# Optimization experiments

Measured on AMD Instinct MI355X. Metric: run time of the kernel, lower is better.

The kernel has to match this reference:

```python
import jax, jax.numpy as jnp
import numpy as np

N = 50000      # nodes
E = 400000     # edges (before self loops)
IN = 128       # in_feat
HID = 64       # n_hidden per head
HEADS = [4, 4, 1]
NEG_SLOPE = 0.2  # DGL GATConv default


def gat_layer(h, src, dst, W, al, ar, b, n_nodes):
    # h: [N, Din]; W: [Din, H*F]; al/ar: [H, F]; b: [H*F]
    H, F = al.shape
    feat = (h @ W).reshape(n_nodes, H, F)              # [N,H,F]
    el = jnp.sum(feat * al, axis=-1)                   # [N,H]
    er = jnp.sum(feat * ar, axis=-1)                   # [N,H]
    e = jax.nn.leaky_relu(el[src] + er[dst], NEG_SLOPE)  # [E,H]
    # edge softmax over destination node segments (stable)
    e_max = jax.lax.stop_gradient(jax.ops.segment_max(e, dst, num_segments=n_nodes))
    ex = jnp.exp(e - e_max[dst])                       # [E,H]
    denom = jax.ops.segment_sum(ex, dst, num_segments=n_nodes)  # [N,H]
    alpha = ex / denom[dst]                            # [E,H]
    msg = feat[src] * alpha[:, :, None]                # [E,H,F]
    out = jax.ops.segment_sum(msg, dst, num_segments=n_nodes)   # [N,H,F]
    out = out + b.reshape(1, H, F)
    return out.reshape(n_nodes, H * F)


def setup_inputs() -> dict:
    key = jax.random.key(0)
    ks = jax.random.split(key, 16)
    inp = {
        "node_feat": jax.random.normal(ks[0], (N, IN), jnp.float32),
        "src": jax.random.randint(ks[1], (E,), 0, N),
        "dst": jax.random.randint(ks[2], (E,), 0, N),
    }
    dins = [IN, HID * HEADS[0], HID * HEADS[1]]
    for i, (din, h) in enumerate(zip(dins, HEADS)):
        k = 3 + 3 * i
        inp[f"W{i}"] = jax.random.normal(ks[k], (din, h * HID), jnp.float32) * 0.1
        inp[f"al{i}"] = jax.random.normal(ks[k + 1], (h, HID), jnp.float32) * 0.1
        inp[f"ar{i}"] = jax.random.normal(ks[k + 2], (h, HID), jnp.float32) * 0.1
        inp[f"b{i}"] = jnp.zeros((h * HID,), jnp.float32)
    return inp


def reference(node_feat, src, dst, W0, al0, ar0, b0, W1, al1, ar1, b1, W2, al2, ar2, b2):
    n_nodes = node_feat.shape[0]
    # add_self_loop
    loop = jnp.arange(n_nodes, dtype=src.dtype)
    src_a = jnp.concatenate([src, loop])
    dst_a = jnp.concatenate([dst, loop])
    h = node_feat
    h = gat_layer(h, src_a, dst_a, W0, al0, ar0, b0, n_nodes)  # [N, 4*64]
    h = gat_layer(h, src_a, dst_a, W1, al1, ar1, b1, n_nodes)  # [N, 4*64]
    h = gat_layer(h, src_a, dst_a, W2, al2, ar2, b2, n_nodes)  # [N, 64]
    return h
```

## Files before the change

### kernel.cpp

```cpp
#include <hip/hip_runtime.h>


typedef __attribute__((ext_vector_type(8))) short short8;
typedef __attribute__((ext_vector_type(4))) float f32x4;

__device__ __forceinline__ float bf2f(ushort u) {
  union { unsigned int i; float f; } c;
  c.i = ((unsigned int)u) << 16;
  return c.f;
}
__device__ __forceinline__ ushort f2bf(float f) {
  union { float f; unsigned int i; } c;
  c.f = f;
  unsigned int u = c.i;
  u += 0x7FFFu + ((u >> 16) & 1u);
  return (ushort)(u >> 16);
}
__device__ __forceinline__ float lrelu_exp(float x) {
  const float y = fmaxf(x, 0.2f * x);
  return __expf(y);
}
__device__ __forceinline__ void gload_lds16(const ushort* g, void* lds) {
  __builtin_amdgcn_global_load_lds(
      (const __attribute__((address_space(1))) unsigned int*)g,
      (__attribute__((address_space(3))) unsigned int*)lds, 16, 0, 0);
}

__global__ __launch_bounds__(256) void cvt_f32_bf16(const float* __restrict__ in,
                                                    ushort* __restrict__ out,
                                                    int n8) {
  const int i = blockIdx.x * 256 + threadIdx.x;
  if (i >= n8) return;
  const float4 v0 = ((const float4*)in)[i * 2];
  const float4 v1 = ((const float4*)in)[i * 2 + 1];
  short8 o;
  o[0] = (short)f2bf(v0.x); o[1] = (short)f2bf(v0.y);
  o[2] = (short)f2bf(v0.z); o[3] = (short)f2bf(v0.w);
  o[4] = (short)f2bf(v1.x); o[5] = (short)f2bf(v1.y);
  o[6] = (short)f2bf(v1.z); o[7] = (short)f2bf(v1.w);
  ((short8*)out)[i] = o;
}

__global__ void convert_w_kernel(const float* __restrict__ W,
                                 ushort* __restrict__ Wt, int K, int N) {
  const int i = blockIdx.x * 256 + threadIdx.x;
  if (i >= K * N) return;
  const int k = i / N, n = i - k * N;
  Wt[n * K + k] = f2bf(W[i]);
}

template <int BN>
__global__ __launch_bounds__(256) void gemm_mfma(
    const ushort* __restrict__ A, const ushort* __restrict__ Wt,
    ushort* __restrict__ C, int M, int K, int Nc) {
  constexpr int NF = BN / 32;
  __shared__ ushort As[128][32];
  __shared__ ushort Bs[BN][32];
  const int bm = blockIdx.x * 128;
  const int bn = blockIdx.y * BN;
  const int tid = threadIdx.x;
  const int lane = tid & 63;
  const int wave = tid >> 6;
  const int wm = wave >> 1;
  const int wn = wave & 1;

  f32x4 acc[4][NF];
#pragma unroll
  for (int m = 0; m < 4; ++m)
#pragma unroll
    for (int n = 0; n < NF; ++n) acc[m][n] = 0.f;

  for (int k0 = 0; k0 < K; k0 += 32) {
#pragma unroll
    for (int c = wave; c < 8; c += 4) {
      const int row = c * 16 + (lane >> 2);
      int rg = bm + row;
      if (rg >= M) rg = M - 1;
      gload_lds16(A + (size_t)rg * K + k0 + (lane & 3) * 8,
                  (char*)(&As[0][0]) + c * 1024);
    }
#pragma unroll
    for (int c = wave; c < BN / 16; c += 4) {
      const int row = c * 16 + (lane >> 2);
      gload_lds16(Wt + (size_t)(bn + row) * K + k0 + (lane & 3) * 8,
                  (char*)(&Bs[0][0]) + c * 1024);
    }
    __syncthreads();

    short8 a[4], b[NF];
#pragma unroll
    for (int m = 0; m < 4; ++m)
      a[m] = *(const short8*)&As[wm * 64 + m * 16 + (lane & 15)][(lane >> 4) * 8];
#pragma unroll
    for (int n = 0; n < NF; ++n)
      b[n] = *(const short8*)&Bs[wn * (NF * 16) + n * 16 + (lane & 15)]
                             [(lane >> 4) * 8];
#pragma unroll
    for (int m = 0; m < 4; ++m)
#pragma unroll
      for (int n = 0; n < NF; ++n)
        acc[m][n] = __builtin_amdgcn_mfma_f32_16x16x32_bf16(a[m], b[n],
                                                            acc[m][n], 0, 0, 0);
    __syncthreads();
  }

#pragma unroll
  for (int m = 0; m < 4; ++m) {
#pragma unroll
    for (int r = 0; r < 4; ++r) {
      const int row = bm + wm * 64 + m * 16 + (lane >> 4) * 4 + r;
      if (row < M) {
#pragma unroll
        for (int n = 0; n < NF; ++n) {
          const int col = bn + wn * (NF * 16) + n * 16 + (lane & 15);
          C[(size_t)row * Nc + col] = f2bf(acc[m][n][r]);
        }
      }
    }
  }
}

__global__ __launch_bounds__(256) void attn_coef_h4(
    const ushort* __restrict__ feat, const float* __restrict__ al,
    const float* __restrict__ ar, float* __restrict__ el,
    float* __restrict__ er, int Nn) {
  if (blockIdx.x == 0 && threadIdx.x < 4) el[Nn * 4 + threadIdx.x] = -1e9f;
  const int n = (blockIdx.x * 256 + threadIdx.x) >> 6;
  const int lane = threadIdx.x & 63;
  if (n >= Nn) return;
  const short4 v = ((const short4*)(feat + (size_t)n * 256))[lane];
  const float4 a = ((const float4*)al)[lane];
  const float4 r = ((const float4*)ar)[lane];
  const float f0 = bf2f((ushort)v.x), f1 = bf2f((ushort)v.y),
              f2 = bf2f((ushort)v.z), f3 = bf2f((ushort)v.w);
  float pl = f0 * a.x + f1 * a.y + f2 * a.z + f3 * a.w;
  float pr = f0 * r.x + f1 * r.y + f2 * r.z + f3 * r.w;
#pragma unroll
  for (int off = 1; off < 16; off <<= 1) {
    pl += __shfl_xor(pl, off);
    pr += __shfl_xor(pr, off);
  }
  if ((lane & 15) == 0) {
    el[n * 4 + (lane >> 4)] = pl;
    er[n * 4 + (lane >> 4)] = pr;
  }
}

__global__ __launch_bounds__(256) void attn_coef_h1(
    const ushort* __restrict__ feat, const float* __restrict__ al,
    const float* __restrict__ ar, float* __restrict__ el,
    float* __restrict__ er, int Nn) {
  if (blockIdx.x == 0 && threadIdx.x == 0) el[Nn] = -1e9f;
  const int wid = (blockIdx.x * 256 + threadIdx.x) >> 6;
  const int lane = threadIdx.x & 63;
  const int n = wid * 4 + (lane >> 4);
  const int sub = lane & 15;
  if (n >= Nn) return;
  const short4 v = ((const short4*)(feat + (size_t)n * 64))[sub];
  const float4 a = ((const float4*)al)[sub];
  const float4 r = ((const float4*)ar)[sub];
  const float f0 = bf2f((ushort)v.x), f1 = bf2f((ushort)v.y),
              f2 = bf2f((ushort)v.z), f3 = bf2f((ushort)v.w);
  float pl = f0 * a.x + f1 * a.y + f2 * a.z + f3 * a.w;
  float pr = f0 * r.x + f1 * r.y + f2 * r.z + f3 * r.w;
#pragma unroll
  for (int off = 1; off < 16; off <<= 1) {
    pl += __shfl_xor(pl, off);
    pr += __shfl_xor(pr, off);
  }
  if (sub == 0) {
    el[n] = pl;
    er[n] = pr;
  }
}

__global__ void hist_kernel(const int* __restrict__ dst, int* __restrict__ cnt,
                            int E, int Nn) {
  const int e = blockIdx.x * blockDim.x + threadIdx.x;
  if (e >= E + Nn) return;
  const int d = (e < E) ? dst[e] : (e - E);
  atomicAdd(&cnt[d], 1);
}

__device__ __forceinline__ int block_incl_scan_1024(int x, int* lds16) {
  const int lane = threadIdx.x & 63;
  const int wid = threadIdx.x >> 6;
  int inc = x;
#pragma unroll
  for (int off = 1; off < 64; off <<= 1) {
    const int y = __shfl_up(inc, off);
    if (lane >= off) inc += y;
  }
  if (lane == 63) lds16[wid] = inc;
  __syncthreads();
  if (wid == 0) {
    int t = (lane < 16) ? lds16[lane] : 0;
#pragma unroll
    for (int off = 1; off < 16; off <<= 1) {
      const int y = __shfl_up(t, off);
      if (lane >= off) t += y;
    }
    if (lane < 16) lds16[lane] = t;
  }
  __syncthreads();
  if (wid > 0) inc += lds16[wid - 1];
  return inc;
}

__global__ __launch_bounds__(1024) void scan_blocks_kernel(
    const int* __restrict__ cnt, int* __restrict__ row_ptr,
    int* __restrict__ partials, int n) {
  __shared__ int lds16[16];
  const int i = blockIdx.x * 1024 + threadIdx.x;
  const int x = (i < n) ? ((cnt[i] + 3) & ~3) : 0;
  const int inc = block_incl_scan_1024(x, lds16);
  if (i < n) row_ptr[i] = inc - x;
  if (threadIdx.x == 1023) partials[blockIdx.x] = inc;
}

__global__ __launch_bounds__(1024) void scan_partials_kernel(
    int* __restrict__ partials, int* __restrict__ row_ptr, int nb, int n) {
  __shared__ int lds16[16];
  const int x = (threadIdx.x < nb) ? partials[threadIdx.x] : 0;
  const int inc = block_incl_scan_1024(x, lds16);
  if (threadIdx.x < nb) partials[threadIdx.x] = inc - x;
  if (threadIdx.x == nb - 1) row_ptr[n] = inc;
}

__global__ __launch_bounds__(1024) void add_offsets_kernel(
    int* __restrict__ row_ptr, int* __restrict__ cursor,
    const int* __restrict__ partials, int n) {
  const int i = blockIdx.x * 1024 + threadIdx.x;
  if (i < n) {
    const int v = row_ptr[i] + partials[blockIdx.x];
    row_ptr[i] = v;
    cursor[i] = v;
  }
}

__global__ void scatter_kernel(const int* __restrict__ src,
                               const int* __restrict__ dst,
                               int* __restrict__ cursor, int* __restrict__ esrc,
                               int E, int Nn) {
  const int e = blockIdx.x * blockDim.x + threadIdx.x;
  if (e >= E + Nn) return;
  const int s = (e < E) ? src[e] : (e - E);
  const int d = (e < E) ? dst[e] : (e - E);
  const int pos = atomicAdd(&cursor[d], 1);
  esrc[pos] = s;
}

__global__ void fill_pad_kernel(const int* __restrict__ cursor,
                                const int* __restrict__ row_ptr,
                                int* __restrict__ esrc, int Nn) {
  const int n = blockIdx.x * 256 + threadIdx.x;
  if (n >= Nn) return;
  const int end = row_ptr[n + 1];
  for (int p = cursor[n]; p < end; ++p) esrc[p] = Nn;
}

__global__ __launch_bounds__(256) void agg_fused_h4(
    const int* __restrict__ row_ptr, const int* __restrict__ esrc,
    const float* __restrict__ el, const float* __restrict__ er,
    const ushort* __restrict__ feat, const float* __restrict__ b,
    ushort* __restrict__ out, int Nn) {
  const int n = (blockIdx.x * 256 + threadIdx.x) >> 6;
  const int lane = threadIdx.x & 63;
  if (n >= Nn) return;
  const int h = lane >> 4;
  const int start = row_ptr[n];
  const int end = row_ptr[n + 1];
  const float erv = er[n * 4 + h];
  const short4* feat4 = (const short4*)feat;

  float den = 0.f;
  f32x4 acc = 0.f;
  for (int i = start; i < end; i += 4) {
    const int s0 = esrc[i], s1 = esrc[i + 1], s2 = esrc[i + 2],
              s3 = esrc[i + 3];
    const float x0 = el[s0 * 4 + h];
    const float x1 = el[s1 * 4 + h];
    const float x2 = el[s2 * 4 + h];
    const float x3 = el[s3 * 4 + h];
    const short4 f0 = feat4[(size_t)s0 * 64 + lane];
    const short4 f1 = feat4[(size_t)s1 * 64 + lane];
    const short4 f2 = feat4[(size_t)s2 * 64 + lane];
    const short4 f3 = feat4[(size_t)s3 * 64 + lane];
    const float e0 = lrelu_exp(x0 + erv), e1 = lrelu_exp(x1 + erv),
                e2 = lrelu_exp(x2 + erv), e3 = lrelu_exp(x3 + erv);
    den += (e0 + e1) + (e2 + e3);
    acc[0] += e0 * bf2f((ushort)f0.x) + e1 * bf2f((ushort)f1.x) +
              e2 * bf2f((ushort)f2.x) + e3 * bf2f((ushort)f3.x);
    acc[1] += e0 * bf2f((ushort)f0.y) + e1 * bf2f((ushort)f1.y) +
              e2 * bf2f((ushort)f2.y) + e3 * bf2f((ushort)f3.y);
    acc[2] += e0 * bf2f((ushort)f0.z) + e1 * bf2f((ushort)f1.z) +
              e2 * bf2f((ushort)f2.z) + e3 * bf2f((ushort)f3.z);
    acc[3] += e0 * bf2f((ushort)f0.w) + e1 * bf2f((ushort)f1.w) +
              e2 * bf2f((ushort)f2.w) + e3 * bf2f((ushort)f3.w);
  }
  const float rden = 1.f / den;
  const float4 bb = ((const float4*)b)[lane];
  short4 o;
  o.x = (short)f2bf(acc[0] * rden + bb.x);
  o.y = (short)f2bf(acc[1] * rden + bb.y);
  o.z = (short)f2bf(acc[2] * rden + bb.z);
  o.w = (short)f2bf(acc[3] * rden + bb.w);
  ((short4*)out)[(size_t)n * 64 + lane] = o;
}

__global__ __launch_bounds__(256) void agg_fused_h1(
    const int* __restrict__ row_ptr, const int* __restrict__ esrc,
    const float* __restrict__ el, const float* __restrict__ er,
    const ushort* __restrict__ feat, const float* __restrict__ b,
    float* __restrict__ out, int Nn) {
  const int wid = (blockIdx.x * 256 + threadIdx.x) >> 6;
  const int lane = threadIdx.x & 63;
  const int n = wid * 2 + (lane >> 5);
  const int sub = lane & 31;
  if (n >= Nn) return;
  const int start = row_ptr[n];
  const int end = row_ptr[n + 1];
  const float erv = er[n];
  const uint* feat2 = (const uint*)feat;

  float den = 0.f;
  float a0 = 0.f, a1 = 0.f;
  for (int i = start; i < end; i += 4) {
    const int s0 = esrc[i], s1 = esrc[i + 1], s2 = esrc[i + 2],
              s3 = esrc[i + 3];
    const float x0 = el[s0], x1 = el[s1], x2 = el[s2], x3 = el[s3];
    const uint f0 = feat2[(size_t)s0 * 32 + sub];
    const uint f1 = feat2[(size_t)s1 * 32 + sub];
    const uint f2 = feat2[(size_t)s2 * 32 + sub];
    const uint f3 = feat2[(size_t)s3 * 32 + sub];
    const float e0 = lrelu_exp(x0 + erv), e1 = lrelu_exp(x1 + erv),
                e2 = lrelu_exp(x2 + erv), e3 = lrelu_exp(x3 + erv);
    den += (e0 + e1) + (e2 + e3);
    a0 += e0 * bf2f((ushort)(f0 & 0xffff)) + e1 * bf2f((ushort)(f1 & 0xffff)) +
          e2 * bf2f((ushort)(f2 & 0xffff)) + e3 * bf2f((ushort)(f3 & 0xffff));
    a1 += e0 * bf2f((ushort)(f0 >> 16)) + e1 * bf2f((ushort)(f1 >> 16)) +
          e2 * bf2f((ushort)(f2 >> 16)) + e3 * bf2f((ushort)(f3 >> 16));
  }
  const float rden = 1.f / den;
  const float2 bb = ((const float2*)b)[sub];
  float2 o;
  o.x = a0 * rden + bb.x;
  o.y = a1 * rden + bb.y;
  ((float2*)out)[(size_t)n * 32 + sub] = o;
}

static void run_layer(const ushort* hin, int K, int H, const float* W,
                      const float* al, const float* ar, const float* b,
                      ushort* Wt, ushort* feat, void* out, float* el,
                      float* er, const int* row_ptr, const int* esrc, int Nn,
                      hipStream_t stream) {
  const int HF = H * 64;
  convert_w_kernel<<<(K * HF + 255) / 256, 256, 0, stream>>>(W, Wt, K, HF);
  if (H == 4) {
    dim3 gg((Nn + 127) / 128, HF / 128);
    gemm_mfma<128><<<gg, 256, 0, stream>>>(hin, Wt, feat, Nn, K, HF);
    const int waves_grid = (Nn * 64 + 255) / 256;
    attn_coef_h4<<<waves_grid, 256, 0, stream>>>(feat, al, ar, el, er, Nn);
    agg_fused_h4<<<waves_grid, 256, 0, stream>>>(row_ptr, esrc, el, er, feat,
                                                 b, (ushort*)out, Nn);
  } else {
    dim3 gg((Nn + 127) / 128, HF / 64);
    gemm_mfma<64><<<gg, 256, 0, stream>>>(hin, Wt, feat, Nn, K, HF);
    attn_coef_h1<<<(Nn * 16 + 255) / 256, 256, 0, stream>>>(feat, al, ar, el,
                                                            er, Nn);
    agg_fused_h1<<<(Nn * 32 + 255) / 256, 256, 0, stream>>>(
        row_ptr, esrc, el, er, feat, b, (float*)out, Nn);
  }
}

extern "C" void kernel_launch(void* const* d_in, const int* in_sizes, int n_in,
                              void* d_out, int out_size, void* d_ws,
                              size_t ws_size, hipStream_t stream) {
  const float* nf = (const float*)d_in[0];
  const int* src = (const int*)d_in[1];
  const int* dst = (const int*)d_in[2];
  const float* W0 = (const float*)d_in[3];
  const float* al0 = (const float*)d_in[4];
  const float* ar0 = (const float*)d_in[5];
  const float* b0 = (const float*)d_in[6];
  const float* W1 = (const float*)d_in[7];
  const float* al1 = (const float*)d_in[8];
  const float* ar1 = (const float*)d_in[9];
  const float* b1 = (const float*)d_in[10];
  const float* W2 = (const float*)d_in[11];
  const float* al2 = (const float*)d_in[12];
  const float* ar2 = (const float*)d_in[13];
  const float* b2 = (const float*)d_in[14];

  const int IN = 128;
  const int Nn = in_sizes[0] / IN;
  const int E = in_sizes[1];
  const int ETP = E + 4 * Nn;

  char* ws = (char*)d_ws;
  size_t off = 0;
  auto alloc = [&](size_t bytes) {
    char* p = ws + off;
    off += (bytes + 255) & ~(size_t)255;
    return p;
  };
  ushort* feat = (ushort*)alloc(((size_t)Nn + 1) * 256 * 2);
  ushort* h1 = (ushort*)alloc((size_t)Nn * 256 * 2);
  ushort* h2 = (ushort*)alloc((size_t)Nn * 256 * 2);
  ushort* a0 = (ushort*)alloc((size_t)Nn * 128 * 2);
  ushort* Wt = (ushort*)alloc((size_t)256 * 256 * 2);
  float* el = (float*)alloc(((size_t)Nn + 1) * 4 * 4);
  float* er = (float*)alloc((size_t)Nn * 4 * 4);
  int* row_ptr = (int*)alloc(((size_t)Nn + 1) * 4);
  int* cnt = (int*)alloc((size_t)Nn * 4);
  int* cursor = (int*)alloc((size_t)Nn * 4);
  int* esrc = (int*)alloc((size_t)ETP * 4);
  int* partials = (int*)alloc((size_t)1024 * 4);
  (void)ws_size;
  (void)n_in;
  (void)out_size;

  hipMemsetAsync(feat + (size_t)Nn * 256, 0, 512, stream);

  cvt_f32_bf16<<<(Nn * 16 + 255) / 256, 256, 0, stream>>>(nf, a0, Nn * 16);

  const int ET = E + Nn;
  const int nb = (Nn + 1023) / 1024;
  hipMemsetAsync(cnt, 0, (size_t)Nn * sizeof(int), stream);
  hist_kernel<<<(ET + 255) / 256, 256, 0, stream>>>(dst, cnt, E, Nn);
  scan_blocks_kernel<<<nb, 1024, 0, stream>>>(cnt, row_ptr, partials, Nn);
  scan_partials_kernel<<<1, 1024, 0, stream>>>(partials, row_ptr, nb, Nn);
  add_offsets_kernel<<<nb, 1024, 0, stream>>>(row_ptr, cursor, partials, Nn);
  scatter_kernel<<<(ET + 255) / 256, 256, 0, stream>>>(src, dst, cursor, esrc,
                                                       E, Nn);
  fill_pad_kernel<<<(Nn + 255) / 256, 256, 0, stream>>>(cursor, row_ptr, esrc,
                                                        Nn);

  run_layer(a0, IN, 4, W0, al0, ar0, b0, Wt, feat, h1, el, er, row_ptr, esrc,
            Nn, stream);
  run_layer(h1, 256, 4, W1, al1, ar1, b1, Wt, feat, h2, el, er, row_ptr, esrc,
            Nn, stream);
  run_layer(h2, 256, 1, W2, al2, ar2, b2, Wt, feat, d_out, el, er, row_ptr,
            esrc, Nn, stream);
}
```

Before: 235.9 us.

## Fuse prep conversions, swizzle GEMM LDS with K=64 tiles, software-pipeline aggregation loads

Merges the node-feature cast and all three weight transposes into one prep kernel, which cuts three separate launches. The GEMM now stages 64-wide K tiles in LDS with an XOR swizzle to reduce bank conflicts and halve the barrier count, at the cost of double the shared memory. The aggregation kernels for H=4 and H=1 prefetch the next group of four neighbours' el and feat values while computing the current group, to hide gather latency at the cost of more registers.

```diff
diff --git a/kernel.cpp b/kernel.cpp
--- a/kernel.cpp
+++ b/kernel.cpp
@@ -26,27 +26,38 @@
       (__attribute__((address_space(3))) unsigned int*)lds, 16, 0, 0);
 }
 
-__global__ __launch_bounds__(256) void cvt_f32_bf16(const float* __restrict__ in,
-                                                    ushort* __restrict__ out,
-                                                    int n8) {
-  const int i = blockIdx.x * 256 + threadIdx.x;
-  if (i >= n8) return;
-  const float4 v0 = ((const float4*)in)[i * 2];
-  const float4 v1 = ((const float4*)in)[i * 2 + 1];
-  short8 o;
-  o[0] = (short)f2bf(v0.x); o[1] = (short)f2bf(v0.y);
-  o[2] = (short)f2bf(v0.z); o[3] = (short)f2bf(v0.w);
-  o[4] = (short)f2bf(v1.x); o[5] = (short)f2bf(v1.y);
-  o[6] = (short)f2bf(v1.z); o[7] = (short)f2bf(v1.w);
-  ((short8*)out)[i] = o;
-}
-
-__global__ void convert_w_kernel(const float* __restrict__ W,
-                                 ushort* __restrict__ Wt, int K, int N) {
-  const int i = blockIdx.x * 256 + threadIdx.x;
-  if (i >= K * N) return;
-  const int k = i / N, n = i - k * N;
-  Wt[n * K + k] = f2bf(W[i]);
+__global__ __launch_bounds__(256) void prep_kernel(
+    const float* __restrict__ nf, ushort* __restrict__ a0, int n8, int nbA,
+    const float* __restrict__ W0, ushort* __restrict__ Wt0,
+    const float* __restrict__ W1, ushort* __restrict__ Wt1,
+    const float* __restrict__ W2, ushort* __restrict__ Wt2) {
+  const int b = blockIdx.x;
+  if (b < nbA) {
+    const int i = b * 256 + threadIdx.x;
+    if (i >= n8) return;
+    const float4 v0 = ((const float4*)nf)[i * 2];
+    const float4 v1 = ((const float4*)nf)[i * 2 + 1];
+    short8 o;
+    o[0] = (short)f2bf(v0.x); o[1] = (short)f2bf(v0.y);
+    o[2] = (short)f2bf(v0.z); o[3] = (short)f2bf(v0.w);
+    o[4] = (short)f2bf(v1.x); o[5] = (short)f2bf(v1.y);
+    o[6] = (short)f2bf(v1.z); o[7] = (short)f2bf(v1.w);
+    ((short8*)a0)[i] = o;
+  } else {
+    const int i = (b - nbA) * 256 + threadIdx.x;
+    if (i < 32768) {
+      const int k = i >> 8, n = i & 255;
+      Wt0[n * 128 + k] = f2bf(W0[i]);
+    } else if (i < 32768 + 65536) {
+      const int j = i - 32768;
+      const int k = j >> 8, n = j & 255;
+      Wt1[n * 256 + k] = f2bf(W1[j]);
+    } else if (i < 32768 + 65536 + 16384) {
+      const int j = i - 32768 - 65536;
+      const int k = j >> 6, n = j & 63;
+      Wt2[n * 256 + k] = f2bf(W2[j]);
+    }
+  }
 }
 
 template <int BN>
@@ -54,8 +65,9 @@
     const ushort* __restrict__ A, const ushort* __restrict__ Wt,
     ushort* __restrict__ C, int M, int K, int Nc) {
   constexpr int NF = BN / 32;
-  __shared__ ushort As[128][32];
-  __shared__ ushort Bs[BN][32];
+  constexpr int NCHB = BN / 8;
+  __shared__ ushort As[128][64];
+  __shared__ ushort Bs[BN][64];
   const int bm = blockIdx.x * 128;
   const int bn = blockIdx.y * BN;
   const int tid = threadIdx.x;
@@ -63,6 +75,8 @@
   const int wave = tid >> 6;
   const int wm = wave >> 1;
   const int wn = wave & 1;
+  const int lrow = lane >> 3;
+  const int lslot = lane & 7;
 
   f32x4 acc[4][NF];
 #pragma unroll
@@ -70,37 +84,47 @@
 #pragma unroll
     for (int n = 0; n < NF; ++n) acc[m][n] = 0.f;
 
-  for (int k0 = 0; k0 < K; k0 += 32) {
-#pragma unroll
-    for (int c = wave; c < 8; c += 4) {
-      const int row = c * 16 + (lane >> 2);
+  for (int k0 = 0; k0 < K; k0 += 64) {
+#pragma unroll
+    for (int c = wave; c < 16; c += 4) {
+      const int row = c * 8 + lrow;
       int rg = bm + row;
       if (rg >= M) rg = M - 1;
-      gload_lds16(A + (size_t)rg * K + k0 + (lane & 3) * 8,
-                  (char*)(&As[0][0]) + c * 1024);
+      const int kcol = (lslot ^ (row & 7)) * 8;
+      gload_lds16(A + (size_t)rg * K + k0 + kcol,
+                  (char*)(&As[0][0]) + c * 1024 + lrow * 128 + lslot * 16);
     }
 #pragma unroll
-    for (int c = wave; c < BN / 16; c += 4) {
-      const int row = c * 16 + (lane >> 2);
-      gload_lds16(Wt + (size_t)(bn + row) * K + k0 + (lane & 3) * 8,
-                  (char*)(&Bs[0][0]) + c * 1024);
+    for (int c = wave; c < NCHB; c += 4) {
+      const int row = c * 8 + lrow;
+      const int kcol = (lslot ^ (row & 7)) * 8;
+      gload_lds16(Wt + (size_t)(bn + row) * K + k0 + kcol,
+                  (char*)(&Bs[0][0]) + c * 1024 + lrow * 128 + lslot * 16);
     }
     __syncthreads();
 
-    short8 a[4], b[NF];
-#pragma unroll
-    for (int m = 0; m < 4; ++m)
-      a[m] = *(const short8*)&As[wm * 64 + m * 16 + (lane & 15)][(lane >> 4) * 8];
-#pragma unroll
-    for (int n = 0; n < NF; ++n)
-      b[n] = *(const short8*)&Bs[wn * (NF * 16) + n * 16 + (lane & 15)]
-                             [(lane >> 4) * 8];
-#pragma unroll
-    for (int m = 0; m < 4; ++m)
-#pragma unroll
-      for (int n = 0; n < NF; ++n)
-        acc[m][n] = __builtin_amdgcn_mfma_f32_16x16x32_bf16(a[m], b[n],
-                                                            acc[m][n], 0, 0, 0);
+#pragma unroll
+    for (int kk = 0; kk < 2; ++kk) {
+      short8 a[4], b[NF];
+#pragma unroll
+      for (int m = 0; m < 4; ++m) {
+        const int row = wm * 64 + m * 16 + (lane & 15);
+        const int slot = (kk * 4 + (lane >> 4)) ^ (row & 7);
+        a[m] = *(const short8*)((const char*)&As[0][0] + row * 128 + slot * 16);
+      }
+#pragma unroll
+      for (int n = 0; n < NF; ++n) {
+        const int row = wn * (NF * 16) + n * 16 + (lane & 15);
+        const int slot = (kk * 4 + (lane >> 4)) ^ (row & 7);
+        b[n] = *(const short8*)((const char*)&Bs[0][0] + row * 128 + slot * 16);
+      }
+#pragma unroll
+      for (int m = 0; m < 4; ++m)
+#pragma unroll
+        for (int n = 0; n < NF; ++n)
+          acc[m][n] = __builtin_amdgcn_mfma_f32_16x16x32_bf16(
+              a[m], b[n], acc[m][n], 0, 0, 0);
+    }
     __syncthreads();
   }
 
@@ -268,24 +292,25 @@
   const int lane = threadIdx.x & 63;
   if (n >= Nn) return;
   const int h = lane >> 4;
-  const int start = row_ptr[n];
+  int i = row_ptr[n];
   const int end = row_ptr[n + 1];
   const float erv = er[n * 4 + h];
-  const short4* feat4 = (const short4*)feat;
+  const short4* fb = (const short4*)feat + lane;
 
   float den = 0.f;
   f32x4 acc = 0.f;
-  for (int i = start; i < end; i += 4) {
-    const int s0 = esrc[i], s1 = esrc[i + 1], s2 = esrc[i + 2],
-              s3 = esrc[i + 3];
-    const float x0 = el[s0 * 4 + h];
-    const float x1 = el[s1 * 4 + h];
-    const float x2 = el[s2 * 4 + h];
-    const float x3 = el[s3 * 4 + h];
-    const short4 f0 = feat4[(size_t)s0 * 64 + lane];
-    const short4 f1 = feat4[(size_t)s1 * 64 + lane];
-    const short4 f2 = feat4[(size_t)s2 * 64 + lane];
-    const short4 f3 = feat4[(size_t)s3 * 64 + lane];
+  int s0 = esrc[i], s1 = esrc[i + 1], s2 = esrc[i + 2], s3 = esrc[i + 3];
+  float x0 = el[s0 * 4 + h], x1 = el[s1 * 4 + h], x2 = el[s2 * 4 + h],
+        x3 = el[s3 * 4 + h];
+  short4 f0 = fb[(size_t)s0 * 64], f1 = fb[(size_t)s1 * 64],
+         f2 = fb[(size_t)s2 * 64], f3 = fb[(size_t)s3 * 64];
+  for (i += 4; i < end; i += 4) {
+    const int t0 = esrc[i], t1 = esrc[i + 1], t2 = esrc[i + 2],
+              t3 = esrc[i + 3];
+    const float y0 = el[t0 * 4 + h], y1 = el[t1 * 4 + h], y2 = el[t2 * 4 + h],
+                y3 = el[t3 * 4 + h];
+    const short4 g0 = fb[(size_t)t0 * 64], g1 = fb[(size_t)t1 * 64],
+                 g2 = fb[(size_t)t2 * 64], g3 = fb[(size_t)t3 * 64];
     const float e0 = lrelu_exp(x0 + erv), e1 = lrelu_exp(x1 + erv),
                 e2 = lrelu_exp(x2 + erv), e3 = lrelu_exp(x3 + erv);
     den += (e0 + e1) + (e2 + e3);
@@ -297,6 +322,21 @@
               e2 * bf2f((ushort)f2.z) + e3 * bf2f((ushort)f3.z);
     acc[3] += e0 * bf2f((ushort)f0.w) + e1 * bf2f((ushort)f1.w) +
               e2 * bf2f((ushort)f2.w) + e3 * bf2f((ushort)f3.w);
+    x0 = y0; x1 = y1; x2 = y2; x3 = y3;
+    f0 = g0; f1 = g1; f2 = g2; f3 = g3;
+  }
+  {
+    const float e0 = lrelu_exp(x0 + erv), e1 = lrelu_exp(x1 + erv),
+                e2 = lrelu_exp(x2 + erv), e3 = lrelu_exp(x3 + erv);
+    den += (e0 + e1) + (e2 + e3);
+    acc[0] += e0 * bf2f((ushort)f0.x) + e1 * bf2f((ushort)f1.x) +
+              e2 * bf2f((ushort)f2.x) + e3 * bf2f((ushort)f3.x);
+    acc[1] += e0 * bf2f((ushort)f0.y) + e1 * bf2f((ushort)f1.y) +
+              e2 * bf2f((ushort)f2.y) + e3 * bf2f((ushort)f3.y);
+    acc[2] += e0 * bf2f((ushort)f0.z) + e1 * bf2f((ushort)f1.z) +
+              e2 * bf2f((ushort)f2.z) + e3 * bf2f((ushort)f3.z);
+    acc[3] += e0 * bf2f((ushort)f0.w) + e1 * bf2f((ushort)f1.w) +
+              e2 * bf2f((ushort)f2.w) + e3 * bf2f((ushort)f3.w);
   }
   const float rden = 1.f / den;
   const float4 bb = ((const float4*)b)[lane];
@@ -318,21 +358,23 @@
   const int n = wid * 2 + (lane >> 5);
   const int sub = lane & 31;
   if (n >= Nn) return;
-  const int start = row_ptr[n];
+  int i = row_ptr[n];
   const int end = row_ptr[n + 1];
   const float erv = er[n];
-  const uint* feat2 = (const uint*)feat;
+  const uint* fb = (const uint*)feat + sub;
 
   float den = 0.f;
   float a0 = 0.f, a1 = 0.f;
-  for (int i = start; i < end; i += 4) {
-    const int s0 = esrc[i], s1 = esrc[i + 1], s2 = esrc[i + 2],
-              s3 = esrc[i + 3];
-    const float x0 = el[s0], x1 = el[s1], x2 = el[s2], x3 = el[s3];
-    const uint f0 = feat2[(size_t)s0 * 32 + sub];
-    const uint f1 = feat2[(size_t)s1 * 32 + sub];
-    const uint f2 = feat2[(size_t)s2 * 32 + sub];
-    const uint f3 = feat2[(size_t)s3 * 32 + sub];
+  int s0 = esrc[i], s1 = esrc[i + 1], s2 = esrc[i + 2], s3 = esrc[i + 3];
+  float x0 = el[s0], x1 = el[s1], x2 = el[s2], x3 = el[s3];
+  uint f0 = fb[(size_t)s0 * 32], f1 = fb[(size_t)s1 * 32],
+       f2 = fb[(size_t)s2 * 32], f3 = fb[(size_t)s3 * 32];
+  for (i += 4; i < end; i += 4) {
+    const int t0 = esrc[i], t1 = esrc[i + 1], t2 = esrc[i + 2],
+              t3 = esrc[i + 3];
+    const float y0 = el[t0], y1 = el[t1], y2 = el[t2], y3 = el[t3];
+    const uint g0 = fb[(size_t)t0 * 32], g1 = fb[(size_t)t1 * 32],
+               g2 = fb[(size_t)t2 * 32], g3 = fb[(size_t)t3 * 32];
     const float e0 = lrelu_exp(x0 + erv), e1 = lrelu_exp(x1 + erv),
                 e2 = lrelu_exp(x2 + erv), e3 = lrelu_exp(x3 + erv);
     den += (e0 + e1) + (e2 + e3);
@@ -340,6 +382,17 @@
           e2 * bf2f((ushort)(f2 & 0xffff)) + e3 * bf2f((ushort)(f3 & 0xffff));
     a1 += e0 * bf2f((ushort)(f0 >> 16)) + e1 * bf2f((ushort)(f1 >> 16)) +
           e2 * bf2f((ushort)(f2 >> 16)) + e3 * bf2f((ushort)(f3 >> 16));
+    x0 = y0; x1 = y1; x2 = y2; x3 = y3;
+    f0 = g0; f1 = g1; f2 = g2; f3 = g3;
+  }
+  {
+    const float e0 = lrelu_exp(x0 + erv), e1 = lrelu_exp(x1 + erv),
+                e2 = lrelu_exp(x2 + erv), e3 = lrelu_exp(x3 + erv);
+    den += (e0 + e1) + (e2 + e3);
+    a0 += e0 * bf2f((ushort)(f0 & 0xffff)) + e1 * bf2f((ushort)(f1 & 0xffff)) +
+          e2 * bf2f((ushort)(f2 & 0xffff)) + e3 * bf2f((ushort)(f3 & 0xffff));
+    a1 += e0 * bf2f((ushort)(f0 >> 16)) + e1 * bf2f((ushort)(f1 >> 16)) +
+          e2 * bf2f((ushort)(f2 >> 16)) + e3 * bf2f((ushort)(f3 >> 16));
   }
   const float rden = 1.f / den;
   const float2 bb = ((const float2*)b)[sub];
@@ -349,13 +402,12 @@
   ((float2*)out)[(size_t)n * 32 + sub] = o;
 }
 
-static void run_layer(const ushort* hin, int K, int H, const float* W,
+static void run_layer(const ushort* hin, int K, int H, const ushort* Wt,
                       const float* al, const float* ar, const float* b,
-                      ushort* Wt, ushort* feat, void* out, float* el,
-                      float* er, const int* row_ptr, const int* esrc, int Nn,
+                      ushort* feat, void* out, float* el, float* er,
+                      const int* row_ptr, const int* esrc, int Nn,
                       hipStream_t stream) {
   const int HF = H * 64;
-  convert_w_kernel<<<(K * HF + 255) / 256, 256, 0, stream>>>(W, Wt, K, HF);
   if (H == 4) {
     dim3 gg((Nn + 127) / 128, HF / 128);
     gemm_mfma<128><<<gg, 256, 0, stream>>>(hin, Wt, feat, Nn, K, HF);
@@ -408,7 +460,9 @@
   ushort* h1 = (ushort*)alloc((size_t)Nn * 256 * 2);
   ushort* h2 = (ushort*)alloc((size_t)Nn * 256 * 2);
   ushort* a0 = (ushort*)alloc((size_t)Nn * 128 * 2);
-  ushort* Wt = (ushort*)alloc((size_t)256 * 256 * 2);
+  ushort* Wt0 = (ushort*)alloc((size_t)256 * 128 * 2);
+  ushort* Wt1 = (ushort*)alloc((size_t)256 * 256 * 2);
+  ushort* Wt2 = (ushort*)alloc((size_t)64 * 256 * 2);
   float* el = (float*)alloc(((size_t)Nn + 1) * 4 * 4);
   float* er = (float*)alloc((size_t)Nn * 4 * 4);
   int* row_ptr = (int*)alloc(((size_t)Nn + 1) * 4);
@@ -422,7 +476,11 @@
 
   hipMemsetAsync(feat + (size_t)Nn * 256, 0, 512, stream);
 
-  cvt_f32_bf16<<<(Nn * 16 + 255) / 256, 256, 0, stream>>>(nf, a0, Nn * 16);
+  const int n8 = Nn * 16;
+  const int nbA = (n8 + 255) / 256;
+  const int nbB = (32768 + 65536 + 16384 + 255) / 256;
+  prep_kernel<<<nbA + nbB, 256, 0, stream>>>(nf, a0, n8, nbA, W0, Wt0, W1, Wt1,
+                                             W2, Wt2);
 
   const int ET = E + Nn;
   const int nb = (Nn + 1023) / 1024;
@@ -436,10 +494,10 @@
   fill_pad_kernel<<<(Nn + 255) / 256, 256, 0, stream>>>(cursor, row_ptr, esrc,
                                                         Nn);
 
-  run_layer(a0, IN, 4, W0, al0, ar0, b0, Wt, feat, h1, el, er, row_ptr, esrc,
+  run_layer(a0, IN, 4, Wt0, al0, ar0, b0, feat, h1, el, er, row_ptr, esrc, Nn,
+            stream);
+  run_layer(h1, 256, 4, Wt1, al1, ar1, b1, feat, h2, el, er, row_ptr, esrc, Nn,
+            stream);
+  run_layer(h2, 256, 1, Wt2, al2, ar2, b2, feat, d_out, el, er, row_ptr, esrc,
             Nn, stream);
-  run_layer(h1, 256, 4, W1, al1, ar1, b1, Wt, feat, h2, el, er, row_ptr, esrc,
-            Nn, stream);
-  run_layer(h2, 256, 1, W2, al2, ar2, b2, Wt, feat, d_out, el, er, row_ptr,
-            esrc, Nn, stream);
-}
+}
```

New measurement: 224.8 us. -4.7%, faster.
